# Optimization experiments

Hardware: AMD Instinct MI355X
Metric: run time of the kernel (lower is better)

Reference implementation:

```python
import jax, jax.numpy as jnp
import numpy as np

N = 2_000_000
F = 32  # feature_num
GH = GW = 256


def _bilinear_interpolate(grid, coords):
    # grid: [H, W, F], coords: [N, 2] in (0,1)
    W = grid.shape[1] - 1
    H = grid.shape[0] - 1
    x = coords[:, 0] * W
    y = coords[:, 1] * H
    x0 = x.astype(jnp.int32)
    y0 = y.astype(jnp.int32)
    xf = x % 1
    yf = y % 1
    x1 = jnp.minimum(x0 + 1, W)
    y1 = jnp.minimum(y0 + 1, H)
    tl = grid[y0, x0]  # [N, F]
    tr = grid[y0, x1]
    bl = grid[y1, x0]
    br = grid[y1, x1]
    top = (1 - xf)[:, None] * tl + xf[:, None] * tr
    bot = (1 - xf)[:, None] * bl + xf[:, None] * br
    return (1 - yf)[:, None] * top + yf[:, None] * bot


def setup_inputs() -> dict:
    key = jax.random.key(0)
    ks = jax.random.split(key, 16)
    inp = {
        "pos": jax.random.uniform(ks[0], (N, 2), dtype=jnp.float32),
        "dir": jax.random.uniform(ks[1], (N, 2), dtype=jnp.float32),
        # grids: randn * 10 as in the torch module
        "pos_grid": jax.random.normal(ks[2], (GH, GW, F), dtype=jnp.float32) * 10.0,
        "dir_grid": jax.random.normal(ks[3], (GH, GW, F), dtype=jnp.float32) * 10.0,
        # shared encoder: Linear(2,4), Linear(4,3)
        "enc_w1": jax.random.normal(ks[4], (2, 4), dtype=jnp.float32) * 0.5,
        "enc_b1": jax.random.normal(ks[5], (4,), dtype=jnp.float32) * 0.1,
        "enc_w2": jax.random.normal(ks[6], (4, 3), dtype=jnp.float32) * 0.5,
        "enc_b2": jax.random.normal(ks[7], (3,), dtype=jnp.float32) * 0.1,
        # fc head: 2F -> 64 -> 16 -> 8 -> 3
        "fc_w1": jax.random.normal(ks[8], (2 * F, 64), dtype=jnp.float32) * 0.1,
        "fc_b1": jnp.zeros((64,), dtype=jnp.float32),
        "fc_w2": jax.random.normal(ks[9], (64, 16), dtype=jnp.float32) * 0.1,
        "fc_b2": jnp.zeros((16,), dtype=jnp.float32),
        "fc_w3": jax.random.normal(ks[10], (16, 8), dtype=jnp.float32) * 0.1,
        "fc_b3": jnp.zeros((8,), dtype=jnp.float32),
        "fc_w4": jax.random.normal(ks[11], (8, 3), dtype=jnp.float32) * 0.1,
        "fc_b4": jnp.zeros((3,), dtype=jnp.float32),
    }
    return inp


def reference(pos, dir, pos_grid, dir_grid,
              enc_w1, enc_b1, enc_w2, enc_b2,
              fc_w1, fc_b1, fc_w2, fc_b2, fc_w3, fc_b3, fc_w4, fc_b4):
    def encoder(x):
        h = jnp.tanh(x @ enc_w1 + enc_b1)
        return jax.nn.sigmoid(h @ enc_w2 + enc_b2)  # [N, 3]; only cols 0,1 used

    p = encoder(pos)
    d = encoder(dir)
    # features are .detach()'ed in the original
    pos_feat = jax.lax.stop_gradient(_bilinear_interpolate(pos_grid, p))
    dir_feat = jax.lax.stop_gradient(_bilinear_interpolate(dir_grid, d))
    x = jnp.concatenate([pos_feat, dir_feat], axis=1)  # [N, 2F]
    # Dropout layers are identity in eval mode
    x = jax.nn.leaky_relu(x @ fc_w1 + fc_b1)
    x = jax.nn.leaky_relu(x @ fc_w2 + fc_b2)
    x = jax.nn.leaky_relu(x @ fc_w3 + fc_b3)
    x = jax.nn.leaky_relu(x @ fc_w4 + fc_b4)
    return jax.nn.sigmoid(x) * 255.0
```

## Files before the change

kernel.cpp:

```cpp
#include <hip/hip_runtime.h>
#include <math.h>

typedef __attribute__((ext_vector_type(8))) __bf16 bf16x8;
typedef __attribute__((ext_vector_type(4))) __bf16 bf16x4;
typedef __attribute__((ext_vector_type(4))) float floatx4;
typedef __attribute__((ext_vector_type(8))) float floatx8;

__device__ __forceinline__ float fast_rcp(float x) { return __builtin_amdgcn_rcpf(x); }
__device__ __forceinline__ float sigmoidf_(float z) { return fast_rcp(1.0f + __expf(-z)); }
__device__ __forceinline__ float fast_tanh(float z) {
    float e = __expf(2.0f * z);
    return 1.0f - 2.0f * fast_rcp(e + 1.0f);
}
__device__ __forceinline__ float leaky(float v) { return fmaxf(v, 0.01f * v); }

__global__ void convert_grids(const float* __restrict__ g0, const float* __restrict__ g1,
                              __bf16* __restrict__ o0, __bf16* __restrict__ o1, int elems) {
    int i = blockIdx.x * blockDim.x + threadIdx.x;
    int nvec = elems >> 2;
    if (i < nvec) {
        float4 v = ((const float4*)g0)[i];
        bf16x4 r = { (__bf16)v.x, (__bf16)v.y, (__bf16)v.z, (__bf16)v.w };
        ((bf16x4*)o0)[i] = r;
    } else if (i < 2 * nvec) {
        int j = i - nvec;
        float4 v = ((const float4*)g1)[j];
        bf16x4 r = { (__bf16)v.x, (__bf16)v.y, (__bf16)v.z, (__bf16)v.w };
        ((bf16x4*)o1)[j] = r;
    }
}

#define XSTR 72

template<bool BF16G>
__global__ __launch_bounds__(256, 3) void gridnet_fwd(
    const float2* __restrict__ pos, const float2* __restrict__ dir_,
    const float* __restrict__ pos_gridf, const float* __restrict__ dir_gridf,
    const __bf16* __restrict__ pos_gridb, const __bf16* __restrict__ dir_gridb,
    const float* __restrict__ enc_w1, const float* __restrict__ enc_b1,
    const float* __restrict__ enc_w2, const float* __restrict__ enc_b2,
    const float* __restrict__ fc_w1, const float* __restrict__ fc_b1,
    const float* __restrict__ fc_w2, const float* __restrict__ fc_b2,
    const float* __restrict__ fc_w3, const float* __restrict__ fc_b3,
    const float* __restrict__ fc_w4, const float* __restrict__ fc_b4,
    float* __restrict__ out, int n)
{
    __shared__ __align__(16) __bf16 smem[4*64*XSTR + 64*XSTR + 16*XSTR];
    __shared__ float b1lds[64];
    __shared__ float b2lds[16];

    const int tid  = threadIdx.x;
    const int lane = tid & 63;
    const int wid  = tid >> 6;
    const int quad = lane >> 4;
    const int l15  = lane & 15;

    __bf16* W1p = smem + 4*64*XSTR;
    __bf16* W2p = W1p + 64*XSTR;
    __bf16* Xw  = smem + wid*64*XSTR;

    for (int idx = tid; idx < 4096; idx += 256)
        W1p[(idx & 63)*XSTR + (idx >> 6)] = (__bf16)fc_w1[idx];
    for (int idx = tid; idx < 1024; idx += 256)
        W2p[(idx & 15)*XSTR + (idx >> 4)] = (__bf16)fc_w2[idx];
    if (tid < 64) b1lds[tid] = fc_b1[tid];
    if (tid < 16) b2lds[tid] = fc_b2[tid];
    __syncthreads();

    floatx4 b1v[4];
    #pragma unroll
    for (int mt = 0; mt < 4; ++mt)
        b1v[mt] = *(const floatx4*)(b1lds + mt*16 + quad*4);
    floatx4 b2v = *(const floatx4*)(b2lds + quad*4);

    int i  = blockIdx.x*256 + wid*64 + lane;
    int ic = min(i, n - 1);

    int   ctl[2], ctr[2], cbl[2], cbr[2];
    float wtl[2], wtr[2], wbl[2], wbr[2];
    #pragma unroll
    for (int pass = 0; pass < 2; ++pass) {
        float2 xy = pass ? dir_[ic] : pos[ic];
        float hh[4];
        #pragma unroll
        for (int k = 0; k < 4; ++k)
            hh[k] = fast_tanh(xy.x*enc_w1[k] + xy.y*enc_w1[4+k] + enc_b1[k]);
        float e0 = enc_b2[0], e1 = enc_b2[1];
        #pragma unroll
        for (int k = 0; k < 4; ++k) {
            e0 += hh[k]*enc_w2[3*k + 0];
            e1 += hh[k]*enc_w2[3*k + 1];
        }
        float x = sigmoidf_(e0) * 255.0f;
        float y = sigmoidf_(e1) * 255.0f;
        int x0 = (int)x, y0 = (int)y;
        float xf = x - (float)x0, yf = y - (float)y0;
        int x1 = min(x0 + 1, 255), y1 = min(y0 + 1, 255);
        float oxf = 1.0f - xf, oyf = 1.0f - yf;
        wtl[pass] = oyf*oxf; wtr[pass] = oyf*xf;
        wbl[pass] = yf*oxf;  wbr[pass] = yf*xf;
        ctl[pass] = ((y0 << 8) + x0) << 5; ctr[pass] = ((y0 << 8) + x1) << 5;
        cbl[pass] = ((y1 << 8) + x0) << 5; cbr[pass] = ((y1 << 8) + x1) << 5;
    }

    #pragma unroll
    for (int pass = 0; pass < 2; ++pass) {
        if (BF16G) {
            const __bf16* g = pass ? dir_gridb : pos_gridb;
            bf16x8 A[4], B[4], C[4], D[4];
            #pragma unroll
            for (int c = 0; c < 4; ++c) A[c] = *(const bf16x8*)(g + ctl[pass] + c*8);
            #pragma unroll
            for (int c = 0; c < 4; ++c) B[c] = *(const bf16x8*)(g + ctr[pass] + c*8);
            #pragma unroll
            for (int c = 0; c < 4; ++c) C[c] = *(const bf16x8*)(g + cbl[pass] + c*8);
            #pragma unroll
            for (int c = 0; c < 4; ++c) D[c] = *(const bf16x8*)(g + cbr[pass] + c*8);
            #pragma unroll
            for (int c = 0; c < 4; ++c) {
                floatx8 r = wtl[pass]*__builtin_convertvector(A[c], floatx8)
                          + wtr[pass]*__builtin_convertvector(B[c], floatx8)
                          + wbl[pass]*__builtin_convertvector(C[c], floatx8)
                          + wbr[pass]*__builtin_convertvector(D[c], floatx8);
                *(bf16x8*)(Xw + lane*XSTR + pass*32 + c*8) = __builtin_convertvector(r, bf16x8);
            }
        } else {
            const float* g = pass ? dir_gridf : pos_gridf;
            #pragma unroll
            for (int c = 0; c < 4; ++c) {
                floatx8 fa = *(const floatx8*)(g + ctl[pass] + c*8);
                floatx8 fb = *(const floatx8*)(g + ctr[pass] + c*8);
                floatx8 fc = *(const floatx8*)(g + cbl[pass] + c*8);
                floatx8 fd = *(const floatx8*)(g + cbr[pass] + c*8);
                floatx8 r = wtl[pass]*fa + wtr[pass]*fb + wbl[pass]*fc + wbr[pass]*fd;
                *(bf16x8*)(Xw + lane*XSTR + pass*32 + c*8) = __builtin_convertvector(r, bf16x8);
            }
        }
    }

    __asm__ volatile("s_waitcnt lgkmcnt(0)" ::: "memory");

    floatx4 acc[4][4];
    #pragma unroll
    for (int mt = 0; mt < 4; ++mt)
        #pragma unroll
        for (int nt = 0; nt < 4; ++nt)
            acc[mt][nt] = b1v[mt];

    #pragma unroll
    for (int ks = 0; ks < 2; ++ks) {
        bf16x8 wf[4], xf[4];
        #pragma unroll
        for (int mt = 0; mt < 4; ++mt)
            wf[mt] = *(const bf16x8*)(W1p + (mt*16 + l15)*XSTR + ks*32 + quad*8);
        #pragma unroll
        for (int nt = 0; nt < 4; ++nt)
            xf[nt] = *(const bf16x8*)(Xw + (nt*16 + l15)*XSTR + ks*32 + quad*8);
        #pragma unroll
        for (int mt = 0; mt < 4; ++mt)
            #pragma unroll
            for (int nt = 0; nt < 4; ++nt)
                acc[mt][nt] = __builtin_amdgcn_mfma_f32_16x16x32_bf16(wf[mt], xf[nt], acc[mt][nt], 0, 0, 0);
    }

    #pragma unroll
    for (int mt = 0; mt < 4; ++mt)
        #pragma unroll
        for (int nt = 0; nt < 4; ++nt) {
            bf16x4 hv;
            #pragma unroll
            for (int r = 0; r < 4; ++r)
                hv[r] = (__bf16)leaky(acc[mt][nt][r]);
            *(bf16x4*)(Xw + (nt*16 + l15)*XSTR + mt*16 + quad*4) = hv;
        }
    __asm__ volatile("s_waitcnt lgkmcnt(0)" ::: "memory");

    floatx4 acc2[4];
    #pragma unroll
    for (int nt = 0; nt < 4; ++nt) acc2[nt] = b2v;
    #pragma unroll
    for (int ks = 0; ks < 2; ++ks) {
        bf16x8 w2f = *(const bf16x8*)(W2p + l15*XSTR + ks*32 + quad*8);
        #pragma unroll
        for (int nt = 0; nt < 4; ++nt) {
            bf16x8 hf = *(const bf16x8*)(Xw + (nt*16 + l15)*XSTR + ks*32 + quad*8);
            acc2[nt] = __builtin_amdgcn_mfma_f32_16x16x32_bf16(w2f, hf, acc2[nt], 0, 0, 0);
        }
    }

    float* H2f = (float*)Xw;
    #pragma unroll
    for (int nt = 0; nt < 4; ++nt) {
        floatx4 hv;
        #pragma unroll
        for (int r = 0; r < 4; ++r)
            hv[r] = leaky(acc2[nt][r]);
        *(floatx4*)(H2f + (nt*16 + l15)*20 + quad*4) = hv;
    }
    __asm__ volatile("s_waitcnt lgkmcnt(0)" ::: "memory");

    float h2[16];
    #pragma unroll
    for (int c = 0; c < 4; ++c) {
        floatx4 v = *(const floatx4*)(H2f + lane*20 + c*4);
        h2[4*c+0] = v[0]; h2[4*c+1] = v[1]; h2[4*c+2] = v[2]; h2[4*c+3] = v[3];
    }
    float h3[8];
    #pragma unroll
    for (int j = 0; j < 8; ++j) h3[j] = fc_b3[j];
    #pragma unroll
    for (int k = 0; k < 16; ++k) {
        float xv = h2[k];
        #pragma unroll
        for (int j = 0; j < 8; ++j) h3[j] = fmaf(xv, fc_w3[(k << 3) + j], h3[j]);
    }
    #pragma unroll
    for (int j = 0; j < 8; ++j) h3[j] = leaky(h3[j]);

    float o[3];
    #pragma unroll
    for (int j = 0; j < 3; ++j) o[j] = fc_b4[j];
    #pragma unroll
    for (int k = 0; k < 8; ++k) {
        float xv = h3[k];
        #pragma unroll
        for (int j = 0; j < 3; ++j) o[j] = fmaf(xv, fc_w4[3*k + j], o[j]);
    }
    if (i < n) {
        #pragma unroll
        for (int j = 0; j < 3; ++j)
            out[3*i + j] = sigmoidf_(leaky(o[j])) * 255.0f;
    }
}

extern "C" void kernel_launch(void* const* d_in, const int* in_sizes, int n_in,
                              void* d_out, int out_size, void* d_ws, size_t ws_size,
                              hipStream_t stream) {
    int n = in_sizes[0] / 2;
    const int GELEMS = 256 * 256 * 32;
    bool use_bf16 = ws_size >= (size_t)(2 * GELEMS * sizeof(__bf16));
    __bf16* g0 = (__bf16*)d_ws;
    __bf16* g1 = g0 + GELEMS;

    if (use_bf16) {
        int total = 2 * (GELEMS / 4);
        convert_grids<<<(total + 255) / 256, 256, 0, stream>>>(
            (const float*)d_in[2], (const float*)d_in[3], g0, g1, GELEMS);
    }

    int blocks = (n + 255) / 256;
    if (use_bf16) {
        gridnet_fwd<true><<<blocks, 256, 0, stream>>>(
            (const float2*)d_in[0], (const float2*)d_in[1],
            (const float*)d_in[2], (const float*)d_in[3], g0, g1,
            (const float*)d_in[4], (const float*)d_in[5],
            (const float*)d_in[6], (const float*)d_in[7],
            (const float*)d_in[8], (const float*)d_in[9],
            (const float*)d_in[10], (const float*)d_in[11],
            (const float*)d_in[12], (const float*)d_in[13],
            (const float*)d_in[14], (const float*)d_in[15],
            (float*)d_out, n);
    } else {
        gridnet_fwd<false><<<blocks, 256, 0, stream>>>(
            (const float2*)d_in[0], (const float2*)d_in[1],
            (const float*)d_in[2], (const float*)d_in[3], g0, g1,
            (const float*)d_in[4], (const float*)d_in[5],
            (const float*)d_in[6], (const float*)d_in[7],
            (const float*)d_in[8], (const float*)d_in[9],
            (const float*)d_in[10], (const float*)d_in[11],
            (const float*)d_in[12], (const float*)d_in[13],
            (const float*)d_in[14], (const float*)d_in[15],
            (float*)d_out, n);
    }
}
```

Before: 235.8 us.

## Pre-transpose FC weights in prep kernel, swizzle LDS, raise occupancy target

The bf16 FC1/FC2 weights are now converted and transposed once in the grid-conversion kernel and read straight from global memory as MFMA fragments, so each block no longer builds a weight copy in LDS. The padded-stride LDS layout becomes an XOR-swizzled 128-byte-row layout to avoid bank conflicts. Launch bounds for the bf16 path ask for 4 blocks per CU. The risks are register pressure from keeping the preloaded weight fragments live, and global or L2 latency on the weight reads.

New measurement: 249.5 us. 5.8% more time.

```diff
diff --git a/kernel.cpp b/kernel.cpp
--- a/kernel.cpp
+++ b/kernel.cpp
@@ -14,8 +14,14 @@
 }
 __device__ __forceinline__ float leaky(float v) { return fmaxf(v, 0.01f * v); }
 
+__device__ __forceinline__ int swzb(int row, int byteoff) {
+    return row * 128 + (byteoff ^ ((row & 7) << 4));
+}
+
 __global__ void convert_grids(const float* __restrict__ g0, const float* __restrict__ g1,
-                              __bf16* __restrict__ o0, __bf16* __restrict__ o1, int elems) {
+                              const float* __restrict__ w1f, const float* __restrict__ w2f,
+                              __bf16* __restrict__ o0, __bf16* __restrict__ o1,
+                              __bf16* __restrict__ w1t, __bf16* __restrict__ w2t, int elems) {
     int i = blockIdx.x * blockDim.x + threadIdx.x;
     int nvec = elems >> 2;
     if (i < nvec) {
@@ -27,16 +33,23 @@
         float4 v = ((const float4*)g1)[j];
         bf16x4 r = { (__bf16)v.x, (__bf16)v.y, (__bf16)v.z, (__bf16)v.w };
         ((bf16x4*)o1)[j] = r;
-    }
-}
-
-#define XSTR 72
+    } else {
+        int j = i - 2 * nvec;
+        if (j < 4096) {
+            w1t[(j & 63) * 64 + (j >> 6)] = (__bf16)w1f[j];
+        } else if (j < 4096 + 1024) {
+            int k = j - 4096;
+            w2t[(k & 15) * 64 + (k >> 4)] = (__bf16)w2f[k];
+        }
+    }
+}
 
 template<bool BF16G>
-__global__ __launch_bounds__(256, 3) void gridnet_fwd(
+__global__ __launch_bounds__(256, BF16G ? 4 : 3) void gridnet_fwd(
     const float2* __restrict__ pos, const float2* __restrict__ dir_,
     const float* __restrict__ pos_gridf, const float* __restrict__ dir_gridf,
     const __bf16* __restrict__ pos_gridb, const __bf16* __restrict__ dir_gridb,
+    const __bf16* __restrict__ W1t, const __bf16* __restrict__ W2t,
     const float* __restrict__ enc_w1, const float* __restrict__ enc_b1,
     const float* __restrict__ enc_w2, const float* __restrict__ enc_b2,
     const float* __restrict__ fc_w1, const float* __restrict__ fc_b1,
@@ -45,7 +58,8 @@
     const float* __restrict__ fc_w4, const float* __restrict__ fc_b4,
     float* __restrict__ out, int n)
 {
-    __shared__ __align__(16) __bf16 smem[4*64*XSTR + 64*XSTR + 16*XSTR];
+    constexpr int XBYTES = 4 * 64 * 128;
+    __shared__ __align__(16) char smem[BF16G ? XBYTES : XBYTES + 64 * 128 + 16 * 128];
     __shared__ float b1lds[64];
     __shared__ float b2lds[16];
 
@@ -55,25 +69,21 @@
     const int quad = lane >> 4;
     const int l15  = lane & 15;
 
-    __bf16* W1p = smem + 4*64*XSTR;
-    __bf16* W2p = W1p + 64*XSTR;
-    __bf16* Xw  = smem + wid*64*XSTR;
-
-    for (int idx = tid; idx < 4096; idx += 256)
-        W1p[(idx & 63)*XSTR + (idx >> 6)] = (__bf16)fc_w1[idx];
-    for (int idx = tid; idx < 1024; idx += 256)
-        W2p[(idx & 15)*XSTR + (idx >> 4)] = (__bf16)fc_w2[idx];
+    char* Xw = smem + wid * 64 * 128;
+    char* W1p = smem + XBYTES;
+    char* W2p = W1p + 64 * 128;
+
+    if (!BF16G) {
+        for (int idx = tid; idx < 4096; idx += 256)
+            *(__bf16*)(W1p + swzb(idx & 63, (idx >> 6) * 2)) = (__bf16)fc_w1[idx];
+        for (int idx = tid; idx < 1024; idx += 256)
+            *(__bf16*)(W2p + swzb(idx & 15, (idx >> 4) * 2)) = (__bf16)fc_w2[idx];
+    }
     if (tid < 64) b1lds[tid] = fc_b1[tid];
     if (tid < 16) b2lds[tid] = fc_b2[tid];
     __syncthreads();
 
-    floatx4 b1v[4];
-    #pragma unroll
-    for (int mt = 0; mt < 4; ++mt)
-        b1v[mt] = *(const floatx4*)(b1lds + mt*16 + quad*4);
-    floatx4 b2v = *(const floatx4*)(b2lds + quad*4);
-
-    int i  = blockIdx.x*256 + wid*64 + lane;
+    int i  = blockIdx.x * 256 + wid * 64 + lane;
     int ic = min(i, n - 1);
 
     int   ctl[2], ctr[2], cbl[2], cbr[2];
@@ -84,12 +94,12 @@
         float hh[4];
         #pragma unroll
         for (int k = 0; k < 4; ++k)
-            hh[k] = fast_tanh(xy.x*enc_w1[k] + xy.y*enc_w1[4+k] + enc_b1[k]);
+            hh[k] = fast_tanh(xy.x * enc_w1[k] + xy.y * enc_w1[4 + k] + enc_b1[k]);
         float e0 = enc_b2[0], e1 = enc_b2[1];
         #pragma unroll
         for (int k = 0; k < 4; ++k) {
-            e0 += hh[k]*enc_w2[3*k + 0];
-            e1 += hh[k]*enc_w2[3*k + 1];
+            e0 += hh[k] * enc_w2[3 * k + 0];
+            e1 += hh[k] * enc_w2[3 * k + 1];
         }
         float x = sigmoidf_(e0) * 255.0f;
         float y = sigmoidf_(e1) * 255.0f;
@@ -97,8 +107,8 @@
         float xf = x - (float)x0, yf = y - (float)y0;
         int x1 = min(x0 + 1, 255), y1 = min(y0 + 1, 255);
         float oxf = 1.0f - xf, oyf = 1.0f - yf;
-        wtl[pass] = oyf*oxf; wtr[pass] = oyf*xf;
-        wbl[pass] = yf*oxf;  wbr[pass] = yf*xf;
+        wtl[pass] = oyf * oxf; wtr[pass] = oyf * xf;
+        wbl[pass] = yf * oxf;  wbr[pass] = yf * xf;
         ctl[pass] = ((y0 << 8) + x0) << 5; ctr[pass] = ((y0 << 8) + x1) << 5;
         cbl[pass] = ((y1 << 8) + x0) << 5; cbr[pass] = ((y1 << 8) + x1) << 5;
     }
@@ -109,36 +119,52 @@
             const __bf16* g = pass ? dir_gridb : pos_gridb;
             bf16x8 A[4], B[4], C[4], D[4];
             #pragma unroll
-            for (int c = 0; c < 4; ++c) A[c] = *(const bf16x8*)(g + ctl[pass] + c*8);
-            #pragma unroll
-            for (int c = 0; c < 4; ++c) B[c] = *(const bf16x8*)(g + ctr[pass] + c*8);
-            #pragma unroll
-            for (int c = 0; c < 4; ++c) C[c] = *(const bf16x8*)(g + cbl[pass] + c*8);
-            #pragma unroll
-            for (int c = 0; c < 4; ++c) D[c] = *(const bf16x8*)(g + cbr[pass] + c*8);
+            for (int c = 0; c < 4; ++c) A[c] = *(const bf16x8*)(g + ctl[pass] + c * 8);
+            #pragma unroll
+            for (int c = 0; c < 4; ++c) B[c] = *(const bf16x8*)(g + ctr[pass] + c * 8);
+            #pragma unroll
+            for (int c = 0; c < 4; ++c) C[c] = *(const bf16x8*)(g + cbl[pass] + c * 8);
+            #pragma unroll
+            for (int c = 0; c < 4; ++c) D[c] = *(const bf16x8*)(g + cbr[pass] + c * 8);
             #pragma unroll
             for (int c = 0; c < 4; ++c) {
-                floatx8 r = wtl[pass]*__builtin_convertvector(A[c], floatx8)
-                          + wtr[pass]*__builtin_convertvector(B[c], floatx8)
-                          + wbl[pass]*__builtin_convertvector(C[c], floatx8)
-                          + wbr[pass]*__builtin_convertvector(D[c], floatx8);
-                *(bf16x8*)(Xw + lane*XSTR + pass*32 + c*8) = __builtin_convertvector(r, bf16x8);
+                floatx8 r = wtl[pass] * __builtin_convertvector(A[c], floatx8)
+                          + wtr[pass] * __builtin_convertvector(B[c], floatx8)
+                          + wbl[pass] * __builtin_convertvector(C[c], floatx8)
+                          + wbr[pass] * __builtin_convertvector(D[c], floatx8);
+                *(bf16x8*)(Xw + swzb(lane, pass * 64 + c * 16)) = __builtin_convertvector(r, bf16x8);
             }
         } else {
             const float* g = pass ? dir_gridf : pos_gridf;
             #pragma unroll
             for (int c = 0; c < 4; ++c) {
-                floatx8 fa = *(const floatx8*)(g + ctl[pass] + c*8);
-                floatx8 fb = *(const floatx8*)(g + ctr[pass] + c*8);
-                floatx8 fc = *(const floatx8*)(g + cbl[pass] + c*8);
-                floatx8 fd = *(const floatx8*)(g + cbr[pass] + c*8);
-                floatx8 r = wtl[pass]*fa + wtr[pass]*fb + wbl[pass]*fc + wbr[pass]*fd;
-                *(bf16x8*)(Xw + lane*XSTR + pass*32 + c*8) = __builtin_convertvector(r, bf16x8);
+                floatx8 fa = *(const floatx8*)(g + ctl[pass] + c * 8);
+                floatx8 fb = *(const floatx8*)(g + ctr[pass] + c * 8);
+                floatx8 fc = *(const floatx8*)(g + cbl[pass] + c * 8);
+                floatx8 fd = *(const floatx8*)(g + cbr[pass] + c * 8);
+                floatx8 r = wtl[pass] * fa + wtr[pass] * fb + wbl[pass] * fc + wbr[pass] * fd;
+                *(bf16x8*)(Xw + swzb(lane, pass * 64 + c * 16)) = __builtin_convertvector(r, bf16x8);
             }
         }
     }
 
     __asm__ volatile("s_waitcnt lgkmcnt(0)" ::: "memory");
+
+    bf16x8 wf[2][4];
+    #pragma unroll
+    for (int ks = 0; ks < 2; ++ks)
+        #pragma unroll
+        for (int mt = 0; mt < 4; ++mt) {
+            if (BF16G)
+                wf[ks][mt] = *(const bf16x8*)(W1t + (mt * 16 + l15) * 64 + ks * 32 + quad * 8);
+            else
+                wf[ks][mt] = *(const bf16x8*)(W1p + swzb(mt * 16 + l15, ks * 64 + quad * 16));
+        }
+
+    floatx4 b1v[4];
+    #pragma unroll
+    for (int mt = 0; mt < 4; ++mt)
+        b1v[mt] = *(const floatx4*)(b1lds + mt * 16 + quad * 4);
 
     floatx4 acc[4][4];
     #pragma unroll
@@ -149,18 +175,15 @@
 
     #pragma unroll
     for (int ks = 0; ks < 2; ++ks) {
-        bf16x8 wf[4], xf[4];
+        bf16x8 xf[4];
+        #pragma unroll
+        for (int nt = 0; nt < 4; ++nt)
+            xf[nt] = *(const bf16x8*)(Xw + swzb(nt * 16 + l15, ks * 64 + quad * 16));
         #pragma unroll
         for (int mt = 0; mt < 4; ++mt)
-            wf[mt] = *(const bf16x8*)(W1p + (mt*16 + l15)*XSTR + ks*32 + quad*8);
-        #pragma unroll
-        for (int nt = 0; nt < 4; ++nt)
-            xf[nt] = *(const bf16x8*)(Xw + (nt*16 + l15)*XSTR + ks*32 + quad*8);
-        #pragma unroll
-        for (int mt = 0; mt < 4; ++mt)
             #pragma unroll
             for (int nt = 0; nt < 4; ++nt)
-                acc[mt][nt] = __builtin_amdgcn_mfma_f32_16x16x32_bf16(wf[mt], xf[nt], acc[mt][nt], 0, 0, 0);
+                acc[mt][nt] = __builtin_amdgcn_mfma_f32_16x16x32_bf16(wf[ks][mt], xf[nt], acc[mt][nt], 0, 0, 0);
     }
 
     #pragma unroll
@@ -171,39 +194,46 @@
             #pragma unroll
             for (int r = 0; r < 4; ++r)
                 hv[r] = (__bf16)leaky(acc[mt][nt][r]);
-            *(bf16x4*)(Xw + (nt*16 + l15)*XSTR + mt*16 + quad*4) = hv;
+            *(bf16x4*)(Xw + swzb(nt * 16 + l15, mt * 32 + quad * 8)) = hv;
         }
     __asm__ volatile("s_waitcnt lgkmcnt(0)" ::: "memory");
 
+    bf16x8 w2f[2];
+    #pragma unroll
+    for (int ks = 0; ks < 2; ++ks) {
+        if (BF16G)
+            w2f[ks] = *(const bf16x8*)(W2t + l15 * 64 + ks * 32 + quad * 8);
+        else
+            w2f[ks] = *(const bf16x8*)(W2p + swzb(l15, ks * 64 + quad * 16));
+    }
+    floatx4 b2v = *(const floatx4*)(b2lds + quad * 4);
     floatx4 acc2[4];
     #pragma unroll
     for (int nt = 0; nt < 4; ++nt) acc2[nt] = b2v;
     #pragma unroll
     for (int ks = 0; ks < 2; ++ks) {
-        bf16x8 w2f = *(const bf16x8*)(W2p + l15*XSTR + ks*32 + quad*8);
         #pragma unroll
         for (int nt = 0; nt < 4; ++nt) {
-            bf16x8 hf = *(const bf16x8*)(Xw + (nt*16 + l15)*XSTR + ks*32 + quad*8);
-            acc2[nt] = __builtin_amdgcn_mfma_f32_16x16x32_bf16(w2f, hf, acc2[nt], 0, 0, 0);
-        }
-    }
-
-    float* H2f = (float*)Xw;
+            bf16x8 hf = *(const bf16x8*)(Xw + swzb(nt * 16 + l15, ks * 64 + quad * 16));
+            acc2[nt] = __builtin_amdgcn_mfma_f32_16x16x32_bf16(w2f[ks], hf, acc2[nt], 0, 0, 0);
+        }
+    }
+
     #pragma unroll
     for (int nt = 0; nt < 4; ++nt) {
         floatx4 hv;
         #pragma unroll
         for (int r = 0; r < 4; ++r)
             hv[r] = leaky(acc2[nt][r]);
-        *(floatx4*)(H2f + (nt*16 + l15)*20 + quad*4) = hv;
+        *(floatx4*)(Xw + swzb(nt * 16 + l15, quad * 16)) = hv;
     }
     __asm__ volatile("s_waitcnt lgkmcnt(0)" ::: "memory");
 
     float h2[16];
     #pragma unroll
     for (int c = 0; c < 4; ++c) {
-        floatx4 v = *(const floatx4*)(H2f + lane*20 + c*4);
-        h2[4*c+0] = v[0]; h2[4*c+1] = v[1]; h2[4*c+2] = v[2]; h2[4*c+3] = v[3];
+        floatx4 v = *(const floatx4*)(Xw + swzb(lane, c * 16));
+        h2[4 * c + 0] = v[0]; h2[4 * c + 1] = v[1]; h2[4 * c + 2] = v[2]; h2[4 * c + 3] = v[3];
     }
     float h3[8];
     #pragma unroll
@@ -224,12 +254,12 @@
     for (int k = 0; k < 8; ++k) {
         float xv = h3[k];
         #pragma unroll
-        for (int j = 0; j < 3; ++j) o[j] = fmaf(xv, fc_w4[3*k + j], o[j]);
+        for (int j = 0; j < 3; ++j) o[j] = fmaf(xv, fc_w4[3 * k + j], o[j]);
     }
     if (i < n) {
         #pragma unroll
         for (int j = 0; j < 3; ++j)
-            out[3*i + j] = sigmoidf_(leaky(o[j])) * 255.0f;
+            out[3 * i + j] = sigmoidf_(leaky(o[j])) * 255.0f;
     }
 }
 
@@ -238,21 +268,26 @@
                               hipStream_t stream) {
     int n = in_sizes[0] / 2;
     const int GELEMS = 256 * 256 * 32;
-    bool use_bf16 = ws_size >= (size_t)(2 * GELEMS * sizeof(__bf16));
-    __bf16* g0 = (__bf16*)d_ws;
-    __bf16* g1 = g0 + GELEMS;
+    const int WELEMS = 4096 + 1024;
+    bool use_bf16 = ws_size >= (size_t)((2 * GELEMS + WELEMS) * sizeof(__bf16));
+    __bf16* g0  = (__bf16*)d_ws;
+    __bf16* g1  = g0 + GELEMS;
+    __bf16* w1t = g1 + GELEMS;
+    __bf16* w2t = w1t + 4096;
 
     if (use_bf16) {
-        int total = 2 * (GELEMS / 4);
+        int total = 2 * (GELEMS / 4) + WELEMS;
         convert_grids<<<(total + 255) / 256, 256, 0, stream>>>(
-            (const float*)d_in[2], (const float*)d_in[3], g0, g1, GELEMS);
+            (const float*)d_in[2], (const float*)d_in[3],
+            (const float*)d_in[8], (const float*)d_in[10],
+            g0, g1, w1t, w2t, GELEMS);
     }
 
     int blocks = (n + 255) / 256;
     if (use_bf16) {
         gridnet_fwd<true><<<blocks, 256, 0, stream>>>(
             (const float2*)d_in[0], (const float2*)d_in[1],
-            (const float*)d_in[2], (const float*)d_in[3], g0, g1,
+            (const float*)d_in[2], (const float*)d_in[3], g0, g1, w1t, w2t,
             (const float*)d_in[4], (const float*)d_in[5],
             (const float*)d_in[6], (const float*)d_in[7],
             (const float*)d_in[8], (const float*)d_in[9],
@@ -263,7 +298,7 @@
     } else {
         gridnet_fwd<false><<<blocks, 256, 0, stream>>>(
             (const float2*)d_in[0], (const float2*)d_in[1],
-            (const float*)d_in[2], (const float*)d_in[3], g0, g1,
+            (const float*)d_in[2], (const float*)d_in[3], g0, g1, w1t, w2t,
             (const float*)d_in[4], (const float*)d_in[5],
             (const float*)d_in[6], (const float*)d_in[7],
             (const float*)d_in[8], (const float*)d_in[9],
```
